# Kernel tuning notes

Measured on AMD Instinct MI355X. Metric: run time of the kernel, lower is better.

The kernel has to match this reference:

```python
import jax, jax.numpy as jnp
import numpy as np

LN_EPS = 1e-5  # torch nn.LayerNorm default


def setup_inputs() -> dict:
    key = jax.random.key(0)
    kx, kw = jax.random.split(key)
    T, B, D = 1024, 8, 2048
    x = jax.random.normal(kx, (T, B, D), dtype=jnp.float32)
    c0 = jnp.zeros((B, D), dtype=jnp.float32)
    # Linear(n_embd, 3*n_embd, bias=False) weight: [3D, D], scaled for sane activations
    W = jax.random.normal(kw, (3 * D, D), dtype=jnp.float32) / np.sqrt(D)
    gamma = jnp.ones((D,), dtype=jnp.float32)
    beta = jnp.zeros((D,), dtype=jnp.float32)
    return {"x": x, "c0": c0, "W": W, "gamma": gamma, "beta": beta}


def reference(x, c0, W, gamma, beta):
    # x: [T, B, D], c0: [B, D], W: [3D, D]
    T, B, D = x.shape
    # Projection for all timesteps at once (same math as per-step Linear).
    ufr = jnp.einsum('tbd,ed->tbe', x, W)  # [T, B, 3D]
    u, f, r = jnp.split(ufr, 3, axis=-1)
    f = jax.nn.sigmoid(f)
    r = jax.nn.sigmoid(r)

    def step(c_prev, inp):
        x_t, u_t, f_t, r_t = inp
        c_t = f_t * c_prev + (1.0 - f_t) * u_t
        h_t = r_t * jnp.tanh(c_t) + (1.0 - r_t) * x_t
        return c_t, h_t

    c_T, h = jax.lax.scan(step, c0, (x, u, f, r))  # h: [T, B, D]

    g = jax.nn.gelu(h, approximate=False)  # torch F.gelu default = exact erf
    mean = jnp.mean(g, axis=-1, keepdims=True)
    var = jnp.var(g, axis=-1, keepdims=True)
    out = (g - mean) * jax.lax.rsqrt(var + LN_EPS) * gamma + beta
    return out, c_T
```

## Files before the change

kernel.cpp:

```cpp
#include <hip/hip_runtime.h>
#include <hip/hip_bf16.h>

#define T_DIM 1024
#define B_DIM 8
#define D_DIM 2048
#define E_DIM 6144
#define N_ROWS 8192
#define K_DIM 2048
#define LN_EPS 1e-5f

#define S2  128
#define CH2 8
#define BD (B_DIM * D_DIM)

typedef short bf16x8 __attribute__((ext_vector_type(8)));
typedef float f32x4 __attribute__((ext_vector_type(4)));
typedef float f32x16 __attribute__((ext_vector_type(16)));

__device__ __forceinline__ unsigned short f2bf(float f) {
  unsigned u = __float_as_uint(f);
  u += 0x7fffu + ((u >> 16) & 1u);
  return (unsigned short)(u >> 16);
}
__device__ __forceinline__ float bf2f(unsigned short h) {
  return __uint_as_float(((unsigned)h) << 16);
}
__device__ __forceinline__ float fast_sigmoid(float x) {
  return __builtin_amdgcn_rcpf(1.f + __expf(-x));
}
__device__ __forceinline__ float fast_tanh(float x) {
  return 1.f - 2.f * __builtin_amdgcn_rcpf(__expf(2.f * x) + 1.f);
}

__global__ __launch_bounds__(256) void cvt_kernel(const float* __restrict__ src,
                                                  unsigned short* __restrict__ dst,
                                                  int n4) {
  int i = blockIdx.x * 256 + threadIdx.x;
  if (i < n4) {
    float4 v = reinterpret_cast<const float4*>(src)[i];
    ushort4 o;
    o.x = f2bf(v.x); o.y = f2bf(v.y); o.z = f2bf(v.z); o.w = f2bf(v.w);
    reinterpret_cast<ushort4*>(dst)[i] = o;
  }
}

#define NT2 32

__global__ __launch_bounds__(512, 2) void gemm8_kernel(
    const unsigned short* __restrict__ A,
    const unsigned short* __restrict__ Bw,
    unsigned short* __restrict__ C) {
  extern __shared__ __align__(16) char smem[];
  const int tid  = threadIdx.x;
  const int lane = tid & 63;
  const int wave = tid >> 6;
  const int wm = wave >> 2;
  const int wn = wave & 3;

  const int bid = blockIdx.x;
  const int tileM = ((bid & 7) * 4 + ((bid >> 3) & 3)) * 256;
  const int tileN = (bid >> 5) * 256;

  const int p0i = wave * 2048 + lane * 16;
  const int p1i = p0i + 1024;
  const int q0i = p0i ^ (((p0i >> 9) & 1) << 5);
  const int q1i = p1i ^ (((p1i >> 9) & 1) << 5);
  const int go0 = ((q0i >> 6) & 127) * 4096 + ((q0i >> 13) << 6) + (q0i & 63);
  const int go1 = ((q1i >> 6) & 127) * 4096 + ((q1i >> 13) << 6) + (q1i & 63);
  const char* Ab = (const char*)A + (size_t)tileM * 4096;
  const char* Bb = (const char*)Bw + (size_t)tileN * 4096;

#define STAGE(kt, h, bufOff)                                                 \
  {                                                                          \
    const char* gs_ = ((h) < 2 ? Ab : Bb) +                                  \
                      (size_t)(((h) & 1) * 128) * 4096 + (size_t)(kt) * 128; \
    char* ds_ = smem + (bufOff) + (h) * 16384 + wave * 2048;                 \
    __builtin_amdgcn_global_load_lds(                                        \
        (const __attribute__((address_space(1))) void*)(gs_ + go0),          \
        (__attribute__((address_space(3))) void*)ds_, 16, 0, 0);             \
    __builtin_amdgcn_global_load_lds(                                        \
        (const __attribute__((address_space(1))) void*)(gs_ + go1),          \
        (__attribute__((address_space(3))) void*)(ds_ + 1024), 16, 0, 0);    \
  }

  const int xbit  = ((lane >> 3) & 1) << 5;
  const int rbase = (lane & 31) * 64 + (lane >> 5) * 16;
  const int aOff  = wm * 16384;
  const int bOff  = 32768 + (wn >> 1) * 16384 + (wn & 1) * 4096;

#define RDA(mi, ks, bufOff)                                                       \
  a[mi][(ks) & 1] = *reinterpret_cast<const bf16x8*>(                             \
      smem + (bufOff) + aOff + (mi) * 2048 + ((ks) >> 1) * 8192 +                 \
      ((rbase + ((ks) & 1) * 32) ^ xbit));
#define RDB(ni, ks, bufOff)                                                       \
  b[ni][(ks) & 1] = *reinterpret_cast<const bf16x8*>(                             \
      smem + (bufOff) + bOff + (ni) * 2048 + ((ks) >> 1) * 8192 +                 \
      ((rbase + ((ks) & 1) * 32) ^ xbit));
#define RD6(ks, bufOff)                                                           \
  RDA(0, ks, bufOff); RDA(1, ks, bufOff); RDA(2, ks, bufOff); RDA(3, ks, bufOff); \
  RDB(0, ks, bufOff); RDB(1, ks, bufOff);
#define MM8(ks)                                                                   \
  acc[0][0] = __builtin_amdgcn_mfma_f32_32x32x16_bf16(a[0][(ks) & 1], b[0][(ks) & 1], acc[0][0], 0, 0, 0); \
  acc[1][0] = __builtin_amdgcn_mfma_f32_32x32x16_bf16(a[1][(ks) & 1], b[0][(ks) & 1], acc[1][0], 0, 0, 0); \
  acc[2][0] = __builtin_amdgcn_mfma_f32_32x32x16_bf16(a[2][(ks) & 1], b[0][(ks) & 1], acc[2][0], 0, 0, 0); \
  acc[3][0] = __builtin_amdgcn_mfma_f32_32x32x16_bf16(a[3][(ks) & 1], b[0][(ks) & 1], acc[3][0], 0, 0, 0); \
  acc[0][1] = __builtin_amdgcn_mfma_f32_32x32x16_bf16(a[0][(ks) & 1], b[1][(ks) & 1], acc[0][1], 0, 0, 0); \
  acc[1][1] = __builtin_amdgcn_mfma_f32_32x32x16_bf16(a[1][(ks) & 1], b[1][(ks) & 1], acc[1][1], 0, 0, 0); \
  acc[2][1] = __builtin_amdgcn_mfma_f32_32x32x16_bf16(a[2][(ks) & 1], b[1][(ks) & 1], acc[2][1], 0, 0, 0); \
  acc[3][1] = __builtin_amdgcn_mfma_f32_32x32x16_bf16(a[3][(ks) & 1], b[1][(ks) & 1], acc[3][1], 0, 0, 0);

  bf16x8 a[4][2], b[2][2];
  f32x16 acc[4][2] = {};

  STAGE(0, 0, 0); STAGE(0, 1, 0); STAGE(0, 2, 0); STAGE(0, 3, 0);
  STAGE(1, 0, 65536); STAGE(1, 1, 65536);
  asm volatile("s_waitcnt vmcnt(4)" ::: "memory");
  __builtin_amdgcn_s_barrier();
  RD6(0, 0);

  for (int j = 0; j < NT2; ++j) {
    const int buf  = (j & 1) << 16;
    const int nbuf = buf ^ 65536;
    asm volatile("s_waitcnt lgkmcnt(0)" ::: "memory");
    __builtin_amdgcn_s_setprio(1);
    if (j < NT2 - 1) STAGE(j + 1, 2, nbuf);
    RD6(1, buf);
    MM8(0);
    __builtin_amdgcn_s_setprio(0);
    __builtin_amdgcn_s_barrier();
    asm volatile("s_waitcnt lgkmcnt(0)" ::: "memory");
    __builtin_amdgcn_s_setprio(1);
    if (j < NT2 - 1) STAGE(j + 1, 3, nbuf);
    RD6(2, buf);
    MM8(1);
    __builtin_amdgcn_s_setprio(0);
    __builtin_amdgcn_s_barrier();
    asm volatile("s_waitcnt lgkmcnt(0)" ::: "memory");
    __builtin_amdgcn_s_setprio(1);
    if (j < NT2 - 2) STAGE(j + 2, 0, buf);
    RD6(3, buf);
    MM8(2);
    __builtin_amdgcn_s_setprio(0);
    __builtin_amdgcn_s_barrier();
    if (j < NT2 - 2) {
      STAGE(j + 2, 1, buf);
      asm volatile("s_waitcnt vmcnt(4)" ::: "memory");
    } else if (j == NT2 - 2) {
      asm volatile("s_waitcnt vmcnt(0)" ::: "memory");
    }
    __builtin_amdgcn_s_barrier();
    __builtin_amdgcn_s_setprio(1);
    RD6(0, nbuf);
    MM8(3);
    __builtin_amdgcn_s_setprio(0);
    __builtin_amdgcn_s_barrier();
  }

  const int ccol = lane & 31;
  const int rb2  = (lane >> 5) * 4;
#pragma unroll
  for (int mi = 0; mi < 4; ++mi) {
#pragma unroll
    for (int ni = 0; ni < 2; ++ni) {
#pragma unroll
      for (int reg = 0; reg < 16; ++reg) {
        int row = tileM + wm * 128 + mi * 32 + (reg & 3) + ((reg >> 2) << 3) + rb2;
        int col = tileN + wn * 64 + ni * 32 + ccol;
        C[(size_t)row * E_DIM + col] = f2bf(acc[mi][ni][reg]);
      }
    }
  }
#undef STAGE
#undef RDA
#undef RDB
#undef RD6
#undef MM8
}

__global__ __launch_bounds__(256) void scan_p1_kernel(
    const unsigned short* __restrict__ ufr,
    float* __restrict__ Aout, float* __restrict__ Bout) {
  const int idx = blockIdx.x * 256 + threadIdx.x;
  const int s = blockIdx.y;
  const int b = idx >> 11;
  const int d = idx & 2047;
  const unsigned short* up =
      ufr + ((size_t)(s * CH2) * B_DIM + b) * E_DIM + d;
  float Aacc = 1.f, Bacc = 0.f;
#pragma unroll
  for (int it = 0; it < CH2; ++it) {
    float u  = bf2f(up[0]);
    float fl = bf2f(up[D_DIM]);
    float f = fast_sigmoid(fl);
    Aacc *= f;
    Bacc = f * Bacc + (1.f - f) * u;
    up += (size_t)B_DIM * E_DIM;
  }
  Aout[(size_t)s * BD + idx] = Aacc;
  Bout[(size_t)s * BD + idx] = Bacc;
}

__global__ __launch_bounds__(256) void scan_p2_kernel(
    const float* __restrict__ c0,
    const float* __restrict__ Ain, const float* __restrict__ Bin,
    float* __restrict__ cs, float* __restrict__ cT) {
  const int idx = blockIdx.x * 256 + threadIdx.x;
  float c = c0[idx];
  for (int s = 0; s < S2; ++s) {
    cs[(size_t)s * BD + idx] = c;
    c = Ain[(size_t)s * BD + idx] * c + Bin[(size_t)s * BD + idx];
  }
  cT[idx] = c;
}

__global__ __launch_bounds__(256) void scan_p3ln_kernel(
    const float* __restrict__ x,
    const unsigned short* __restrict__ ufr,
    const float* __restrict__ cs,
    const float* __restrict__ gamma,
    const float* __restrict__ beta,
    float* __restrict__ out) {
  const int b = blockIdx.x & (B_DIM - 1);
  const int s = blockIdx.x >> 3;
  const int tid = threadIdx.x;
  const int lane = tid & 63;
  const int wave = tid >> 6;
  const int d0 = tid * 8;
  __shared__ float red[8];

  float c[8];
  {
    const float* csp = cs + (size_t)s * BD + b * D_DIM + d0;
    float4 v0 = *(const float4*)csp;
    float4 v1 = *(const float4*)(csp + 4);
    c[0]=v0.x; c[1]=v0.y; c[2]=v0.z; c[3]=v0.w;
    c[4]=v1.x; c[5]=v1.y; c[6]=v1.z; c[7]=v1.w;
  }
  float gam[8], bet[8];
  {
    float4 g0 = *(const float4*)(gamma + d0);
    float4 g1 = *(const float4*)(gamma + d0 + 4);
    float4 b0 = *(const float4*)(beta + d0);
    float4 b1 = *(const float4*)(beta + d0 + 4);
    gam[0]=g0.x; gam[1]=g0.y; gam[2]=g0.z; gam[3]=g0.w;
    gam[4]=g1.x; gam[5]=g1.y; gam[6]=g1.z; gam[7]=g1.w;
    bet[0]=b0.x; bet[1]=b0.y; bet[2]=b0.z; bet[3]=b0.w;
    bet[4]=b1.x; bet[5]=b1.y; bet[6]=b1.z; bet[7]=b1.w;
  }

  for (int it = 0; it < CH2; ++it) {
    const size_t rowo = (size_t)(s * CH2 + it) * B_DIM + b;
    const unsigned short* up = ufr + rowo * E_DIM + d0;
    const float* xp = x + rowo * D_DIM + d0;
    ushort4 uv0 = *(const ushort4*)up;
    ushort4 uv1 = *(const ushort4*)(up + 4);
    ushort4 fv0 = *(const ushort4*)(up + D_DIM);
    ushort4 fv1 = *(const ushort4*)(up + D_DIM + 4);
    ushort4 rv0 = *(const ushort4*)(up + 2 * D_DIM);
    ushort4 rv1 = *(const ushort4*)(up + 2 * D_DIM + 4);
    float4 xv0 = *(const float4*)xp;
    float4 xv1 = *(const float4*)(xp + 4);
    unsigned short uu[8] = {uv0.x, uv0.y, uv0.z, uv0.w, uv1.x, uv1.y, uv1.z, uv1.w};
    unsigned short ff[8] = {fv0.x, fv0.y, fv0.z, fv0.w, fv1.x, fv1.y, fv1.z, fv1.w};
    unsigned short rr[8] = {rv0.x, rv0.y, rv0.z, rv0.w, rv1.x, rv1.y, rv1.z, rv1.w};
    float xx[8] = {xv0.x, xv0.y, xv0.z, xv0.w, xv1.x, xv1.y, xv1.z, xv1.w};

    float g[8];
    float s1 = 0.f, sq = 0.f;
#pragma unroll
    for (int jj = 0; jj < 8; ++jj) {
      float f = fast_sigmoid(bf2f(ff[jj]));
      float r = fast_sigmoid(bf2f(rr[jj]));
      c[jj] = f * c[jj] + (1.f - f) * bf2f(uu[jj]);
      float h = r * fast_tanh(c[jj]) + (1.f - r) * xx[jj];
      float gg = 0.5f * h * (1.f + erff(h * 0.70710678118654752f));
      g[jj] = gg;
      s1 += gg;
      sq += gg * gg;
    }
#pragma unroll
    for (int off = 32; off; off >>= 1) {
      s1 += __shfl_xor(s1, off);
      sq += __shfl_xor(sq, off);
    }
    if (lane == 0) { red[wave] = s1; red[4 + wave] = sq; }
    __syncthreads();
    float S1 = red[0] + red[1] + red[2] + red[3];
    float Sq = red[4] + red[5] + red[6] + red[7];
    __syncthreads();
    float mean = S1 * (1.f / D_DIM);
    float var  = Sq * (1.f / D_DIM) - mean * mean;
    float inv = rsqrtf(var + LN_EPS);

    float* op = out + rowo * D_DIM + d0;
    float4 o0 = {(g[0] - mean) * inv * gam[0] + bet[0],
                 (g[1] - mean) * inv * gam[1] + bet[1],
                 (g[2] - mean) * inv * gam[2] + bet[2],
                 (g[3] - mean) * inv * gam[3] + bet[3]};
    float4 o1 = {(g[4] - mean) * inv * gam[4] + bet[4],
                 (g[5] - mean) * inv * gam[5] + bet[5],
                 (g[6] - mean) * inv * gam[6] + bet[6],
                 (g[7] - mean) * inv * gam[7] + bet[7]};
    *(float4*)op = o0;
    *(float4*)(op + 4) = o1;
  }
}

extern "C" void kernel_launch(void* const* d_in, const int* in_sizes, int n_in,
                              void* d_out, int out_size, void* d_ws, size_t ws_size,
                              hipStream_t stream) {
  const float* x     = (const float*)d_in[0];
  const float* c0    = (const float*)d_in[1];
  const float* W     = (const float*)d_in[2];
  const float* gamma = (const float*)d_in[3];
  const float* beta  = (const float*)d_in[4];
  float* out = (float*)d_out;
  float* cT  = out + (size_t)N_ROWS * D_DIM;

  unsigned short* ufr = (unsigned short*)d_ws;
  unsigned short* xb  = ufr + (size_t)N_ROWS * E_DIM;
  unsigned short* wb  = xb + (size_t)N_ROWS * K_DIM;

  float* Abuf = (float*)xb;
  float* Bbuf = Abuf + (size_t)S2 * BD;
  float* csb  = Bbuf + (size_t)S2 * BD;

  int nx4 = N_ROWS * K_DIM / 4;
  int nw4 = E_DIM * K_DIM / 4;
  cvt_kernel<<<(nx4 + 255) / 256, 256, 0, stream>>>(x, xb, nx4);
  cvt_kernel<<<(nw4 + 255) / 256, 256, 0, stream>>>(W, wb, nw4);

  (void)hipFuncSetAttribute((const void*)gemm8_kernel,
                            hipFuncAttributeMaxDynamicSharedMemorySize, 131072);
  gemm8_kernel<<<768, 512, 131072, stream>>>(xb, wb, ufr);

  dim3 sg(BD / 256, S2);
  scan_p1_kernel<<<sg, 256, 0, stream>>>(ufr, Abuf, Bbuf);
  scan_p2_kernel<<<BD / 256, 256, 0, stream>>>(c0, Abuf, Bbuf, csb, cT);
  scan_p3ln_kernel<<<B_DIM * S2, 256, 0, stream>>>(x, ufr, csb, gamma, beta, out);
}
```

Before: 286.3 us.

## Re-layout GEMM LDS tiles with row-XOR swizzle and reorder MFMA phases

Changes the LDS layout of the bf16 GEMM tiles to 128-byte rows with an XOR swizzle on 16-byte cells, and rewrites the LDS-read addressing to match. The inner loop is restructured so that A fragments for all four k-steps are held in registers and MFMAs are grouped by N-subtile. The explicit lgkmcnt waits are dropped and the global-to-LDS staging of the next tile is moved into a different phase. The aim is fewer LDS bank conflicts and better overlap of LDS reads with MFMA. In exchange it raises register pressure under the 512x2 launch bound, and removing the waits relies on compiler-inserted synchronization.

```diff
diff --git a/kernel.cpp b/kernel.cpp
--- a/kernel.cpp
+++ b/kernel.cpp
@@ -63,10 +63,10 @@
 
   const int p0i = wave * 2048 + lane * 16;
   const int p1i = p0i + 1024;
-  const int q0i = p0i ^ (((p0i >> 9) & 1) << 5);
-  const int q1i = p1i ^ (((p1i >> 9) & 1) << 5);
-  const int go0 = ((q0i >> 6) & 127) * 4096 + ((q0i >> 13) << 6) + (q0i & 63);
-  const int go1 = ((q1i >> 6) & 127) * 4096 + ((q1i >> 13) << 6) + (q1i & 63);
+  const int r0i = p0i >> 7;
+  const int r1i = p1i >> 7;
+  const int go0 = r0i * 4096 + ((p0i & 127) ^ ((r0i & 7) << 4));
+  const int go1 = r1i * 4096 + ((p1i & 127) ^ ((r1i & 7) << 4));
   const char* Ab = (const char*)A + (size_t)tileM * 4096;
   const char* Bb = (const char*)Bw + (size_t)tileN * 4096;
 
@@ -83,63 +83,57 @@
         (__attribute__((address_space(3))) void*)(ds_ + 1024), 16, 0, 0);    \
   }
 
-  const int xbit  = ((lane >> 3) & 1) << 5;
-  const int rbase = (lane & 31) * 64 + (lane >> 5) * 16;
-  const int aOff  = wm * 16384;
-  const int bOff  = 32768 + (wn >> 1) * 16384 + (wn & 1) * 4096;
-
-#define RDA(mi, ks, bufOff)                                                       \
-  a[mi][(ks) & 1] = *reinterpret_cast<const bf16x8*>(                             \
-      smem + (bufOff) + aOff + (mi) * 2048 + ((ks) >> 1) * 8192 +                 \
-      ((rbase + ((ks) & 1) * 32) ^ xbit));
-#define RDB(ni, ks, bufOff)                                                       \
-  b[ni][(ks) & 1] = *reinterpret_cast<const bf16x8*>(                             \
-      smem + (bufOff) + bOff + (ni) * 2048 + ((ks) >> 1) * 8192 +                 \
-      ((rbase + ((ks) & 1) * 32) ^ xbit));
-#define RD6(ks, bufOff)                                                           \
-  RDA(0, ks, bufOff); RDA(1, ks, bufOff); RDA(2, ks, bufOff); RDA(3, ks, bufOff); \
-  RDB(0, ks, bufOff); RDB(1, ks, bufOff);
-#define MM8(ks)                                                                   \
-  acc[0][0] = __builtin_amdgcn_mfma_f32_32x32x16_bf16(a[0][(ks) & 1], b[0][(ks) & 1], acc[0][0], 0, 0, 0); \
-  acc[1][0] = __builtin_amdgcn_mfma_f32_32x32x16_bf16(a[1][(ks) & 1], b[0][(ks) & 1], acc[1][0], 0, 0, 0); \
-  acc[2][0] = __builtin_amdgcn_mfma_f32_32x32x16_bf16(a[2][(ks) & 1], b[0][(ks) & 1], acc[2][0], 0, 0, 0); \
-  acc[3][0] = __builtin_amdgcn_mfma_f32_32x32x16_bf16(a[3][(ks) & 1], b[0][(ks) & 1], acc[3][0], 0, 0, 0); \
-  acc[0][1] = __builtin_amdgcn_mfma_f32_32x32x16_bf16(a[0][(ks) & 1], b[1][(ks) & 1], acc[0][1], 0, 0, 0); \
-  acc[1][1] = __builtin_amdgcn_mfma_f32_32x32x16_bf16(a[1][(ks) & 1], b[1][(ks) & 1], acc[1][1], 0, 0, 0); \
-  acc[2][1] = __builtin_amdgcn_mfma_f32_32x32x16_bf16(a[2][(ks) & 1], b[1][(ks) & 1], acc[2][1], 0, 0, 0); \
-  acc[3][1] = __builtin_amdgcn_mfma_f32_32x32x16_bf16(a[3][(ks) & 1], b[1][(ks) & 1], acc[3][1], 0, 0, 0);
-
-  bf16x8 a[4][2], b[2][2];
+  const int rlo  = (lane & 31) * 128;
+  const int kg   = lane >> 5;
+  const int sw   = lane & 7;
+  const int aOff = wm * 16384;
+  const int bOff = 32768 + (wn >> 1) * 16384 + (wn & 1) * 8192;
+
+#define CELL(ks) ((((((ks) << 1) | kg) ^ sw)) << 4)
+#define RDA(mi, ks, bufOff)                                                    \
+  a[mi][ks] = *reinterpret_cast<const bf16x8*>(                                \
+      smem + (bufOff) + aOff + (mi) * 4096 + rlo + CELL(ks));
+#define RDB(ni, ks, bufOff)                                                    \
+  b[ni][ks] = *reinterpret_cast<const bf16x8*>(                                \
+      smem + (bufOff) + bOff + (ni) * 4096 + rlo + CELL(ks));
+#define MM1(mi, ni, ks)                                                        \
+  acc[mi][ni] = __builtin_amdgcn_mfma_f32_32x32x16_bf16(a[mi][ks], b[ni][ks],  \
+                                                        acc[mi][ni], 0, 0, 0);
+#define MMQ(ni, ka, kb)                                                        \
+  MM1(0, ni, ka) MM1(1, ni, ka) MM1(2, ni, ka) MM1(3, ni, ka)                  \
+  MM1(0, ni, kb) MM1(1, ni, kb) MM1(2, ni, kb) MM1(3, ni, kb)
+
+  bf16x8 a[4][4], b[2][4];
   f32x16 acc[4][2] = {};
 
   STAGE(0, 0, 0); STAGE(0, 1, 0); STAGE(0, 2, 0); STAGE(0, 3, 0);
   STAGE(1, 0, 65536); STAGE(1, 1, 65536);
   asm volatile("s_waitcnt vmcnt(4)" ::: "memory");
   __builtin_amdgcn_s_barrier();
-  RD6(0, 0);
+  RDA(0, 0, 0); RDA(1, 0, 0); RDA(2, 0, 0); RDA(3, 0, 0);
+  RDA(0, 1, 0); RDA(1, 1, 0); RDA(2, 1, 0); RDA(3, 1, 0);
+  RDB(0, 0, 0); RDB(0, 1, 0);
 
   for (int j = 0; j < NT2; ++j) {
     const int buf  = (j & 1) << 16;
     const int nbuf = buf ^ 65536;
-    asm volatile("s_waitcnt lgkmcnt(0)" ::: "memory");
     __builtin_amdgcn_s_setprio(1);
-    if (j < NT2 - 1) STAGE(j + 1, 2, nbuf);
-    RD6(1, buf);
-    MM8(0);
+    RDA(0, 2, buf); RDA(1, 2, buf); RDA(2, 2, buf); RDA(3, 2, buf);
+    RDA(0, 3, buf); RDA(1, 3, buf); RDA(2, 3, buf); RDA(3, 3, buf);
+    RDB(0, 2, buf); RDB(0, 3, buf);
+    MMQ(0, 0, 1);
     __builtin_amdgcn_s_setprio(0);
     __builtin_amdgcn_s_barrier();
-    asm volatile("s_waitcnt lgkmcnt(0)" ::: "memory");
     __builtin_amdgcn_s_setprio(1);
-    if (j < NT2 - 1) STAGE(j + 1, 3, nbuf);
-    RD6(2, buf);
-    MM8(1);
+    if (j < NT2 - 1) { STAGE(j + 1, 2, nbuf); STAGE(j + 1, 3, nbuf); }
+    RDB(1, 0, buf); RDB(1, 1, buf);
+    MMQ(0, 2, 3);
     __builtin_amdgcn_s_setprio(0);
     __builtin_amdgcn_s_barrier();
-    asm volatile("s_waitcnt lgkmcnt(0)" ::: "memory");
     __builtin_amdgcn_s_setprio(1);
     if (j < NT2 - 2) STAGE(j + 2, 0, buf);
-    RD6(3, buf);
-    MM8(2);
+    RDB(1, 2, buf); RDB(1, 3, buf);
+    MMQ(1, 0, 1);
     __builtin_amdgcn_s_setprio(0);
     __builtin_amdgcn_s_barrier();
     if (j < NT2 - 2) {
@@ -150,8 +144,12 @@
     }
     __builtin_amdgcn_s_barrier();
     __builtin_amdgcn_s_setprio(1);
-    RD6(0, nbuf);
-    MM8(3);
+    if (j < NT2 - 1) {
+      RDA(0, 0, nbuf); RDA(1, 0, nbuf); RDA(2, 0, nbuf); RDA(3, 0, nbuf);
+      RDA(0, 1, nbuf); RDA(1, 1, nbuf); RDA(2, 1, nbuf); RDA(3, 1, nbuf);
+      RDB(0, 0, nbuf); RDB(0, 1, nbuf);
+    }
+    MMQ(1, 2, 3);
     __builtin_amdgcn_s_setprio(0);
     __builtin_amdgcn_s_barrier();
   }
@@ -171,10 +169,11 @@
     }
   }
 #undef STAGE
+#undef CELL
 #undef RDA
 #undef RDB
-#undef RD6
-#undef MM8
+#undef MM1
+#undef MMQ
 }
 
 __global__ __launch_bounds__(256) void scan_p1_kernel(
```

After: 287.6 us. No clear change (+0.5%).
